# Optimization experiments

Hardware: AMD Instinct MI355X
Metric: run time of the kernel (lower is better)

## Reference

```python
import jax, jax.numpy as jnp
import numpy as np

B, N, F_IN = 32, 1024, 128
DIM, NUM_HEAD = 16, 8
D = DIM * NUM_HEAD  # 128


def setup_inputs() -> dict:
    key = jax.random.key(0)
    ks = jax.random.split(key, 8)
    atom_query = jax.random.normal(ks[0], (B, N, F_IN), dtype=jnp.float32)
    mask = (jax.random.uniform(ks[1], (B, N, 1)) < 0.9).astype(jnp.float32)
    s = 1.0 / np.sqrt(F_IN)
    Wq = jax.random.normal(ks[2], (F_IN, D), dtype=jnp.float32) * s
    bq = jnp.zeros((D,), dtype=jnp.float32)
    Wk = jax.random.normal(ks[3], (F_IN, D), dtype=jnp.float32) * s
    bk = jnp.zeros((D,), dtype=jnp.float32)
    Wv = jax.random.normal(ks[4], (F_IN, D), dtype=jnp.float32) * s
    bv = jnp.zeros((D,), dtype=jnp.float32)
    return {"atom_query": atom_query, "mask": mask,
            "Wq": Wq, "bq": bq, "Wk": Wk, "bk": bk, "Wv": Wv, "bv": bv}


def reference(atom_query, mask, Wq, bq, Wk, bk, Wv, bv):
    scale = 0.5  # self.scale
    q = atom_query @ Wq + bq            # [B, N, D]
    k = atom_query @ Wk + bk            # [B, N, D]
    v = atom_query @ Wv + bv            # [B, N, D] (v_proj=True)
    dk = jnp.asarray(q.shape[-1], jnp.float32) ** (-scale)
    q = q * dk
    energy = jnp.einsum('bqd,bkd->bqk', q, k)      # [B, N, N]
    energy = mask * energy                          # mask broadcasts over k
    agg = jnp.sum(energy, axis=-1, keepdims=True)   # [B, N, 1]
    agg = mask * agg
    # norm=False branch skipped
    agg = agg + (1.0 - mask) * (-1e9)
    attn = jax.nn.softmax(agg, axis=1)              # softmax over query axis
    context = jnp.sum(mask * (attn * v), axis=1)    # [B, D]
    return attn, context
```

## Files before the change

### kernel.cpp

```cpp
#include <hip/hip_runtime.h>

#define B   32
#define N   1024
#define FIN 128
#define DD  128
#define CH  8
#define ROWS 128

#define OFF_PASUM 0
#define OFF_AGG   32768
#define OFF_WPART 65536
#define OFF_MPART 98304
#define OFF_LPART 98560
#define OFF_SPART 98816
#define OFF_U     99072
#define OFF_C     103168

__global__ __launch_bounds__(256) void k_asum(const float* __restrict__ aq,
                                              float* __restrict__ ws) {
    const int b = blockIdx.x >> 3, ch = blockIdx.x & 7;
    const int f4 = threadIdx.x & 31;
    const int g  = threadIdx.x >> 5;
    const float4* aq4 = (const float4*)aq + (size_t)(b * N + ch * ROWS) * 32;
    float4 acc = make_float4(0.f, 0.f, 0.f, 0.f);
    for (int j = 0; j < 16; ++j) {
        const int n = g + 8 * j;
        float4 v = aq4[n * 32 + f4];
        acc.x += v.x; acc.y += v.y; acc.z += v.z; acc.w += v.w;
    }
    __shared__ float4 sh[256];
    sh[threadIdx.x] = acc;
    __syncthreads();
    if (threadIdx.x < 32) {
        float4 r = sh[threadIdx.x];
        for (int gg = 1; gg < 8; ++gg) {
            float4 t = sh[gg * 32 + threadIdx.x];
            r.x += t.x; r.y += t.y; r.z += t.z; r.w += t.w;
        }
        float4* outp = (float4*)(ws + OFF_PASUM) + (b * CH + ch) * 32;
        outp[threadIdx.x] = r;
    }
}

__global__ __launch_bounds__(128) void k_prep(const float* __restrict__ Wq,
                                              const float* __restrict__ bq,
                                              const float* __restrict__ Wk,
                                              const float* __restrict__ bk,
                                              float* __restrict__ ws) {
    const int b = blockIdx.x, t = threadIdx.x;
    __shared__ float asum[FIN], ksum[DD];
    float a = 0.f;
    for (int ch = 0; ch < CH; ++ch) a += ws[OFF_PASUM + (b * CH + ch) * FIN + t];
    asum[t] = a;
    __syncthreads();
    float ks = 1024.0f * bk[t];
    for (int f = 0; f < FIN; ++f) ks += asum[f] * Wk[f * DD + t];
    ksum[t] = ks;
    __syncthreads();
    float uu = 0.f;
    for (int d = 0; d < DD; ++d) uu += Wq[t * DD + d] * ksum[d];
    ws[OFF_U + b * FIN + t] = uu;
    if (t == 0) {
        float cc = 0.f;
        for (int d = 0; d < DD; ++d) cc += bq[d] * ksum[d];
        ws[OFF_C + b] = cc;
    }
}

__global__ __launch_bounds__(256) void k_agg(const float* __restrict__ aq,
                                             const float* __restrict__ mask,
                                             float* __restrict__ ws) {
    const int b = blockIdx.x >> 3, ch = blockIdx.x & 7;
    const int tid = threadIdx.x, lane = tid & 63, w = tid >> 6;
    __shared__ float u_s[FIN];
    __shared__ float sh_m[4], sh_l[4], sh_s[4], sh_w[4 * FIN];
    if (tid < FIN) u_s[tid] = ws[OFF_U + b * FIN + tid];
    const float c_b = ws[OFF_C + b];
    __syncthreads();

    const float dk = 0.08838834764831845f;
    float mw = -1e30f, lw = 0.f, sacc = 0.f, w0 = 0.f, w1 = 0.f;
    const int n0 = ch * ROWS + w * 32;
    const float* aqb = aq + (size_t)b * N * FIN;
    for (int r = 0; r < 32; ++r) {
        const int n = n0 + r;
        const float a0 = aqb[n * FIN + lane];
        const float a1 = aqb[n * FIN + 64 + lane];
        float v = a0 * u_s[lane] + a1 * u_s[lane + 64];
        for (int off = 32; off > 0; off >>= 1) v += __shfl_xor(v, off);
        const float m = mask[b * N + n];
        const float raw = dk * (v + c_b);
        const float aggv = m * raw + (1.0f - m) * (-1e9f);
        if (lane == 0) ws[OFF_AGG + b * N + n] = aggv;
        const float nm = fmaxf(mw, aggv);
        const float sc = __expf(mw - nm);
        const float p  = __expf(aggv - nm);
        const float mp = m * p;
        lw   = lw * sc + p;
        sacc = sacc * sc + mp;
        w0   = w0 * sc + mp * a0;
        w1   = w1 * sc + mp * a1;
        mw = nm;
    }
    if (lane == 0) { sh_m[w] = mw; sh_l[w] = lw; sh_s[w] = sacc; }
    sh_w[w * FIN + lane]      = w0;
    sh_w[w * FIN + 64 + lane] = w1;
    __syncthreads();
    if (tid < FIN) {
        const float M = fmaxf(fmaxf(sh_m[0], sh_m[1]), fmaxf(sh_m[2], sh_m[3]));
        const float e0 = __expf(sh_m[0] - M), e1 = __expf(sh_m[1] - M);
        const float e2 = __expf(sh_m[2] - M), e3 = __expf(sh_m[3] - M);
        ws[OFF_WPART + (b * CH + ch) * FIN + tid] =
            e0 * sh_w[tid] + e1 * sh_w[FIN + tid] + e2 * sh_w[2 * FIN + tid] + e3 * sh_w[3 * FIN + tid];
        if (tid == 0) {
            ws[OFF_MPART + b * CH + ch] = M;
            ws[OFF_LPART + b * CH + ch] = e0 * sh_l[0] + e1 * sh_l[1] + e2 * sh_l[2] + e3 * sh_l[3];
            ws[OFF_SPART + b * CH + ch] = e0 * sh_s[0] + e1 * sh_s[1] + e2 * sh_s[2] + e3 * sh_s[3];
        }
    }
}

__global__ __launch_bounds__(256) void k_final(const float* __restrict__ Wv,
                                               const float* __restrict__ bv,
                                               const float* __restrict__ ws,
                                               float* __restrict__ out) {
    const int b = blockIdx.x, tid = threadIdx.x;
    float mv[CH];
    float M = -1e30f;
    for (int ch = 0; ch < CH; ++ch) {
        mv[ch] = ws[OFF_MPART + b * CH + ch];
        M = fmaxf(M, mv[ch]);
    }
    float E[CH], L = 0.f, S = 0.f;
    for (int ch = 0; ch < CH; ++ch) {
        E[ch] = __expf(mv[ch] - M);
        L += E[ch] * ws[OFF_LPART + b * CH + ch];
        S += E[ch] * ws[OFF_SPART + b * CH + ch];
    }
    __shared__ float wsh[FIN];
    if (tid < FIN) {
        float wf = 0.f;
        for (int ch = 0; ch < CH; ++ch) wf += E[ch] * ws[OFF_WPART + (b * CH + ch) * FIN + tid];
        wsh[tid] = wf;
    }
    __syncthreads();
    const float invL = 1.0f / L;
    if (tid < FIN) {
        float ctx = 0.f;
        for (int f = 0; f < FIN; ++f) ctx += wsh[f] * Wv[f * DD + tid];
        out[B * N + b * DD + tid] = ctx * invL + S * invL * bv[tid];
    }
    for (int j = 0; j < 4; ++j) {
        const int n = j * 256 + tid;
        out[b * N + n] = __expf(ws[OFF_AGG + b * N + n] - M) * invL;
    }
}

extern "C" void kernel_launch(void* const* d_in, const int* in_sizes, int n_in,
                              void* d_out, int out_size, void* d_ws, size_t ws_size,
                              hipStream_t stream) {
    const float* aq   = (const float*)d_in[0];
    const float* mask = (const float*)d_in[1];
    const float* Wq   = (const float*)d_in[2];
    const float* bq   = (const float*)d_in[3];
    const float* Wk   = (const float*)d_in[4];
    const float* bk   = (const float*)d_in[5];
    const float* Wv   = (const float*)d_in[6];
    const float* bv   = (const float*)d_in[7];
    float* ws  = (float*)d_ws;
    float* out = (float*)d_out;

    k_asum <<<B * CH, 256, 0, stream>>>(aq, ws);
    k_prep <<<B,      128, 0, stream>>>(Wq, bq, Wk, bk, ws);
    k_agg  <<<B * CH, 256, 0, stream>>>(aq, mask, ws);
    k_final<<<B,      256, 0, stream>>>(Wv, bv, ws, out);
}
```

Baseline: 106.0 us.

## Fuse four kernels into one cooperative kernel with LDS-resident input tile

Replaces the four separate launches with a single cooperative kernel that uses grid-wide syncs between phases. Each block loads its 64-row slice of atom_query once into a swizzled shared-memory tile. That tile is reused for the column sum, the per-row dot product and the weighted sum, so the input is read from global memory once instead of twice. The per-block projection work is redundantly recomputed by every chunk block, and the chunk count is doubled to 16. This adds two grid syncs, a larger shared-memory footprint, and the requirement that all 512 blocks be co-resident.

```diff
diff --git a/kernel.cpp b/kernel.cpp
--- a/kernel.cpp
+++ b/kernel.cpp
@@ -1,158 +1,194 @@
 #include <hip/hip_runtime.h>
-
-#define B   32
-#define N   1024
-#define FIN 128
-#define DD  128
-#define CH  8
-#define ROWS 128
+#include <hip/hip_cooperative_groups.h>
+
+namespace cg = cooperative_groups;
+
+#define B    32
+#define N    1024
+#define FIN  128
+#define CHN  16
+#define ROWS 64
+#define GRID (B * CHN)
 
 #define OFF_PASUM 0
-#define OFF_AGG   32768
-#define OFF_WPART 65536
-#define OFF_MPART 98304
-#define OFF_LPART 98560
-#define OFF_SPART 98816
-#define OFF_U     99072
-#define OFF_C     103168
-
-__global__ __launch_bounds__(256) void k_asum(const float* __restrict__ aq,
-                                              float* __restrict__ ws) {
-    const int b = blockIdx.x >> 3, ch = blockIdx.x & 7;
-    const int f4 = threadIdx.x & 31;
-    const int g  = threadIdx.x >> 5;
-    const float4* aq4 = (const float4*)aq + (size_t)(b * N + ch * ROWS) * 32;
-    float4 acc = make_float4(0.f, 0.f, 0.f, 0.f);
-    for (int j = 0; j < 16; ++j) {
-        const int n = g + 8 * j;
-        float4 v = aq4[n * 32 + f4];
-        acc.x += v.x; acc.y += v.y; acc.z += v.z; acc.w += v.w;
-    }
-    __shared__ float4 sh[256];
-    sh[threadIdx.x] = acc;
-    __syncthreads();
-    if (threadIdx.x < 32) {
-        float4 r = sh[threadIdx.x];
-        for (int gg = 1; gg < 8; ++gg) {
-            float4 t = sh[gg * 32 + threadIdx.x];
-            r.x += t.x; r.y += t.y; r.z += t.z; r.w += t.w;
-        }
-        float4* outp = (float4*)(ws + OFF_PASUM) + (b * CH + ch) * 32;
-        outp[threadIdx.x] = r;
-    }
-}
-
-__global__ __launch_bounds__(128) void k_prep(const float* __restrict__ Wq,
-                                              const float* __restrict__ bq,
-                                              const float* __restrict__ Wk,
-                                              const float* __restrict__ bk,
-                                              float* __restrict__ ws) {
-    const int b = blockIdx.x, t = threadIdx.x;
-    __shared__ float asum[FIN], ksum[DD];
-    float a = 0.f;
-    for (int ch = 0; ch < CH; ++ch) a += ws[OFF_PASUM + (b * CH + ch) * FIN + t];
-    asum[t] = a;
-    __syncthreads();
-    float ks = 1024.0f * bk[t];
-    for (int f = 0; f < FIN; ++f) ks += asum[f] * Wk[f * DD + t];
-    ksum[t] = ks;
-    __syncthreads();
-    float uu = 0.f;
-    for (int d = 0; d < DD; ++d) uu += Wq[t * DD + d] * ksum[d];
-    ws[OFF_U + b * FIN + t] = uu;
-    if (t == 0) {
-        float cc = 0.f;
-        for (int d = 0; d < DD; ++d) cc += bq[d] * ksum[d];
-        ws[OFF_C + b] = cc;
-    }
-}
-
-__global__ __launch_bounds__(256) void k_agg(const float* __restrict__ aq,
-                                             const float* __restrict__ mask,
-                                             float* __restrict__ ws) {
-    const int b = blockIdx.x >> 3, ch = blockIdx.x & 7;
-    const int tid = threadIdx.x, lane = tid & 63, w = tid >> 6;
-    __shared__ float u_s[FIN];
-    __shared__ float sh_m[4], sh_l[4], sh_s[4], sh_w[4 * FIN];
-    if (tid < FIN) u_s[tid] = ws[OFF_U + b * FIN + tid];
-    const float c_b = ws[OFF_C + b];
-    __syncthreads();
-
-    const float dk = 0.08838834764831845f;
-    float mw = -1e30f, lw = 0.f, sacc = 0.f, w0 = 0.f, w1 = 0.f;
-    const int n0 = ch * ROWS + w * 32;
-    const float* aqb = aq + (size_t)b * N * FIN;
-    for (int r = 0; r < 32; ++r) {
-        const int n = n0 + r;
-        const float a0 = aqb[n * FIN + lane];
-        const float a1 = aqb[n * FIN + 64 + lane];
-        float v = a0 * u_s[lane] + a1 * u_s[lane + 64];
-        for (int off = 32; off > 0; off >>= 1) v += __shfl_xor(v, off);
-        const float m = mask[b * N + n];
-        const float raw = dk * (v + c_b);
-        const float aggv = m * raw + (1.0f - m) * (-1e9f);
-        if (lane == 0) ws[OFF_AGG + b * N + n] = aggv;
-        const float nm = fmaxf(mw, aggv);
-        const float sc = __expf(mw - nm);
-        const float p  = __expf(aggv - nm);
-        const float mp = m * p;
-        lw   = lw * sc + p;
-        sacc = sacc * sc + mp;
-        w0   = w0 * sc + mp * a0;
-        w1   = w1 * sc + mp * a1;
-        mw = nm;
-    }
-    if (lane == 0) { sh_m[w] = mw; sh_l[w] = lw; sh_s[w] = sacc; }
-    sh_w[w * FIN + lane]      = w0;
-    sh_w[w * FIN + 64 + lane] = w1;
-    __syncthreads();
+#define OFF_WPART (B * CHN * FIN)
+#define OFF_M     (2 * B * CHN * FIN)
+#define OFF_L     (OFF_M + B * CHN)
+#define OFF_S     (OFF_L + B * CHN)
+
+__global__ __launch_bounds__(256, 2) void k_fused(
+    const float* __restrict__ aq, const float* __restrict__ mask,
+    const float* __restrict__ Wq, const float* __restrict__ bq,
+    const float* __restrict__ Wk, const float* __restrict__ bk,
+    const float* __restrict__ Wv, const float* __restrict__ bv,
+    float* __restrict__ ws, float* __restrict__ out)
+{
+    cg::grid_group grid = cg::this_grid();
+    const int b = blockIdx.x >> 4, ch = blockIdx.x & 15;
+    const int tid = threadIdx.x;
+    const int f = tid & 127, h = tid >> 7;
+
+    __shared__ float tile[ROWS * FIN];
+    __shared__ float red[256], red2[256];
+    __shared__ float asum_s[FIN], ksum_s[FIN], u_s[FIN];
+    __shared__ float mp_s[ROWS];
+
+    {
+        const float4* g4 = (const float4*)aq + ((size_t)b * N + ch * ROWS) * 32;
+        float4* t4 = (float4*)tile;
+        #pragma unroll
+        for (int i = 0; i < 8; ++i) {
+            int g = i * 256 + tid;
+            int row = g >> 5, c4 = g & 31;
+            t4[row * 32 + (c4 ^ (row & 31))] = g4[g];
+        }
+    }
+    __syncthreads();
+    {
+        float acc = 0.f;
+        #pragma unroll 8
+        for (int i = 0; i < 32; ++i) {
+            int r = h * 32 + i;
+            acc += tile[r * FIN + ((((f >> 2) ^ (r & 31)) << 2) | (f & 3))];
+        }
+        red[tid] = acc;
+        __syncthreads();
+        if (tid < FIN)
+            ws[OFF_PASUM + (b * CHN + ch) * FIN + f] = red[f] + red[f + 128];
+    }
+    __threadfence();
+    grid.sync();
+
     if (tid < FIN) {
-        const float M = fmaxf(fmaxf(sh_m[0], sh_m[1]), fmaxf(sh_m[2], sh_m[3]));
-        const float e0 = __expf(sh_m[0] - M), e1 = __expf(sh_m[1] - M);
-        const float e2 = __expf(sh_m[2] - M), e3 = __expf(sh_m[3] - M);
-        ws[OFF_WPART + (b * CH + ch) * FIN + tid] =
-            e0 * sh_w[tid] + e1 * sh_w[FIN + tid] + e2 * sh_w[2 * FIN + tid] + e3 * sh_w[3 * FIN + tid];
+        float a = 0.f;
+        #pragma unroll
+        for (int c = 0; c < CHN; ++c)
+            a += ws[OFF_PASUM + (b * CHN + c) * FIN + f];
+        asum_s[f] = a;
+    }
+    __syncthreads();
+    {
+        float ks = 0.f;
+        #pragma unroll 8
+        for (int i = 0; i < 64; ++i) {
+            int fi = h * 64 + i;
+            ks += asum_s[fi] * Wk[fi * FIN + f];
+        }
+        red[tid] = ks;
+        __syncthreads();
+        if (tid < FIN) ksum_s[f] = red[f] + red[f + 128] + 1024.f * bk[f];
+        __syncthreads();
+    }
+    float c_b;
+    {
+        float uu = 0.f;
+        #pragma unroll 8
+        for (int i = 0; i < 64; ++i) {
+            int d = h * 64 + i;
+            uu += Wq[f * FIN + d] * ksum_s[d];
+        }
+        red[tid] = uu;
+        red2[tid] = (h == 0) ? bq[f] * ksum_s[f] : 0.f;
+        __syncthreads();
+        if (tid < FIN) u_s[f] = red[f] + red[f + 128];
+        for (int s = 128; s > 0; s >>= 1) {
+            if (tid < s) red2[tid] += red2[tid + s];
+            __syncthreads();
+        }
+        c_b = red2[0];
+    }
+
+    const float dkc = 0.08838834764831845f;
+    float aggv = -1e30f;
+    {
+        const int r = tid & 63, q = tid >> 6;
+        const float4* t4 = (const float4*)tile;
+        const float4* u4 = (const float4*)u_s;
+        float acc = 0.f;
+        #pragma unroll
+        for (int jj = 0; jj < 8; ++jj) {
+            int j = q * 8 + jj;
+            float4 a = t4[r * 32 + (j ^ (r & 31))];
+            float4 uu = u4[j];
+            acc += a.x * uu.x + a.y * uu.y + a.z * uu.z + a.w * uu.w;
+        }
+        red[tid] = acc;
+    }
+    __syncthreads();
+    if (tid < ROWS) {
+        float dot = red[tid] + red[tid + 64] + red[tid + 128] + red[tid + 192];
+        float m = mask[b * N + ch * ROWS + tid];
+        float raw = dkc * (dot + c_b);
+        aggv = m * raw + (1.f - m) * (-1e9f);
+        float Mc = aggv;
+        #pragma unroll
+        for (int off = 32; off > 0; off >>= 1)
+            Mc = fmaxf(Mc, __shfl_xor(Mc, off));
+        float p = __expf(aggv - Mc);
+        float mp = m * p;
+        mp_s[tid] = mp;
+        float Lc = p, Sc = mp;
+        #pragma unroll
+        for (int off = 32; off > 0; off >>= 1) {
+            Lc += __shfl_xor(Lc, off);
+            Sc += __shfl_xor(Sc, off);
+        }
         if (tid == 0) {
-            ws[OFF_MPART + b * CH + ch] = M;
-            ws[OFF_LPART + b * CH + ch] = e0 * sh_l[0] + e1 * sh_l[1] + e2 * sh_l[2] + e3 * sh_l[3];
-            ws[OFF_SPART + b * CH + ch] = e0 * sh_s[0] + e1 * sh_s[1] + e2 * sh_s[2] + e3 * sh_s[3];
-        }
-    }
-}
-
-__global__ __launch_bounds__(256) void k_final(const float* __restrict__ Wv,
-                                               const float* __restrict__ bv,
-                                               const float* __restrict__ ws,
-                                               float* __restrict__ out) {
-    const int b = blockIdx.x, tid = threadIdx.x;
-    float mv[CH];
-    float M = -1e30f;
-    for (int ch = 0; ch < CH; ++ch) {
-        mv[ch] = ws[OFF_MPART + b * CH + ch];
-        M = fmaxf(M, mv[ch]);
-    }
-    float E[CH], L = 0.f, S = 0.f;
-    for (int ch = 0; ch < CH; ++ch) {
-        E[ch] = __expf(mv[ch] - M);
-        L += E[ch] * ws[OFF_LPART + b * CH + ch];
-        S += E[ch] * ws[OFF_SPART + b * CH + ch];
-    }
-    __shared__ float wsh[FIN];
-    if (tid < FIN) {
-        float wf = 0.f;
-        for (int ch = 0; ch < CH; ++ch) wf += E[ch] * ws[OFF_WPART + (b * CH + ch) * FIN + tid];
-        wsh[tid] = wf;
-    }
-    __syncthreads();
-    const float invL = 1.0f / L;
-    if (tid < FIN) {
+            ws[OFF_M + b * CHN + ch] = Mc;
+            ws[OFF_L + b * CHN + ch] = Lc;
+            ws[OFF_S + b * CHN + ch] = Sc;
+        }
+    }
+    __syncthreads();
+    {
+        float w = 0.f;
+        #pragma unroll 8
+        for (int i = 0; i < 32; ++i) {
+            int r = h * 32 + i;
+            w += mp_s[r] * tile[r * FIN + ((((f >> 2) ^ (r & 31)) << 2) | (f & 3))];
+        }
+        red[tid] = w;
+        __syncthreads();
+        if (tid < FIN)
+            ws[OFF_WPART + (b * CHN + ch) * FIN + f] = red[f] + red[f + 128];
+    }
+    __threadfence();
+    grid.sync();
+
+    float M = -3.0e38f;
+    #pragma unroll
+    for (int c = 0; c < CHN; ++c)
+        M = fmaxf(M, ws[OFF_M + b * CHN + c]);
+    float Em[CHN], L = 0.f, S = 0.f;
+    #pragma unroll
+    for (int c = 0; c < CHN; ++c) {
+        float e = __expf(ws[OFF_M + b * CHN + c] - M);
+        Em[c] = e;
+        L += e * ws[OFF_L + b * CHN + c];
+        S += e * ws[OFF_S + b * CHN + c];
+    }
+    const float invL = 1.f / L;
+    if (tid < ROWS)
+        out[b * N + ch * ROWS + tid] = __expf(aggv - M) * invL;
+    if (ch == 0) {
+        if (tid < FIN) {
+            float w = 0.f;
+            #pragma unroll
+            for (int c = 0; c < CHN; ++c)
+                w += Em[c] * ws[OFF_WPART + (b * CHN + c) * FIN + f];
+            u_s[f] = w;
+        }
+        __syncthreads();
         float ctx = 0.f;
-        for (int f = 0; f < FIN; ++f) ctx += wsh[f] * Wv[f * DD + tid];
-        out[B * N + b * DD + tid] = ctx * invL + S * invL * bv[tid];
-    }
-    for (int j = 0; j < 4; ++j) {
-        const int n = j * 256 + tid;
-        out[b * N + n] = __expf(ws[OFF_AGG + b * N + n] - M) * invL;
+        #pragma unroll 8
+        for (int i = 0; i < 64; ++i) {
+            int fi = h * 64 + i;
+            ctx += u_s[fi] * Wv[fi * FIN + f];
+        }
+        red[tid] = ctx;
+        __syncthreads();
+        if (tid < FIN)
+            out[B * N + b * FIN + f] = (red[f] + red[f + 128]) * invL + S * invL * bv[f];
     }
 }
 
@@ -170,8 +206,8 @@
     float* ws  = (float*)d_ws;
     float* out = (float*)d_out;
 
-    k_asum <<<B * CH, 256, 0, stream>>>(aq, ws);
-    k_prep <<<B,      128, 0, stream>>>(Wq, bq, Wk, bk, ws);
-    k_agg  <<<B * CH, 256, 0, stream>>>(aq, mask, ws);
-    k_final<<<B,      256, 0, stream>>>(Wv, bv, ws, out);
+    void* args[] = {(void*)&aq, (void*)&mask, (void*)&Wq, (void*)&bq, (void*)&Wk,
+                    (void*)&bk, (void*)&Wv, (void*)&bv, (void*)&ws, (void*)&out};
+    hipLaunchCooperativeKernel((const void*)k_fused, dim3(GRID), dim3(256),
+                               args, 0, stream);
 }
```

After: 253.1 us. 139% more time.
